# Kernel tuning notes

Hardware: AMD Instinct MI355X
Metric: run time of the kernel (lower is better)

The kernel has to match this reference:

```python
import jax, jax.numpy as jnp
import numpy as np

# Ternary quant: brevitas 2-bit narrow-range signed int quant with const scale 1.0
# -> q(x) = clamp(round(x), -1, 1), values in {-1, 0, 1}

def ternary(x):
    return jnp.clip(jnp.round(x), -1.0, 1.0)

def batchnorm(x, gamma, beta, eps=1e-5):
    # training-mode BatchNorm1d: batch statistics over dim 0 (biased var)
    mean = jnp.mean(x, axis=0)
    var = jnp.var(x, axis=0)
    return (x - mean) * jax.lax.rsqrt(var + eps) * gamma + beta

def tensornorm(x, w, b, eps=1e-4):
    # BNN-PYNQ TensorNorm: normalize over whole tensor (unbiased var), scalar affine
    mean = jnp.mean(x)
    var = jnp.var(x, ddof=1)
    return (x - mean) / jnp.sqrt(var + eps) * w + b


def setup_inputs() -> dict:
    key = jax.random.key(0)
    ks = jax.random.split(key, 4)
    B = 16384
    x = jax.random.uniform(ks[0], (B, 784), dtype=jnp.float32)          # MNIST-like in [0,1]
    W1 = 2.0 * jax.random.uniform(ks[1], (1024, 784), dtype=jnp.float32) - 1.0  # uniform(-1,1)
    W2 = 2.0 * jax.random.uniform(ks[2], (10, 1024), dtype=jnp.float32) - 1.0
    tnk1, tnk2 = jax.random.split(ks[3])
    return {
        "x": x,
        "W1": W1,
        "gamma1": jnp.ones((1024,), jnp.float32),
        "beta1": jnp.zeros((1024,), jnp.float32),
        "W2": W2,
        "gamma2": jnp.ones((10,), jnp.float32),
        "beta2": jnp.zeros((10,), jnp.float32),
        "tn_w": jax.random.uniform(tnk1, (1,), dtype=jnp.float32),
        "tn_b": jax.random.uniform(tnk2, (1,), dtype=jnp.float32),
    }


def reference(x, W1, gamma1, beta1, W2, gamma2, beta2, tn_w, tn_b):
    h = x.reshape(x.shape[0], -1)
    h = 2.0 * h - 1.0                 # input rescale to [-1,1]
    h = ternary(h)                    # QuantIdentity (2-bit act)
    h = h @ ternary(W1).T             # QuantLinear 784->1024, ternary weights, no bias
    h = batchnorm(h, gamma1, beta1)   # BatchNorm1d(1024)
    h = ternary(h)                    # QuantIdentity
    h = h @ ternary(W2).T             # QuantLinear 1024->10
    h = batchnorm(h, gamma2, beta2)   # BatchNorm1d(10)
    h = ternary(h)                    # QuantIdentity
    return tensornorm(h, tn_w, tn_b)  # TensorNorm
```

## Files before the change

### kernel.cpp

```cpp
#include <hip/hip_runtime.h>
#include <stdint.h>

typedef int i32x4 __attribute__((ext_vector_type(4)));
typedef short s16x8 __attribute__((ext_vector_type(8)));
typedef unsigned long long ull;

#define BB 16384
#define KD 784
#define KP 832
#define N1 1024
#define N2 10
#define NTOT (BB * N2)

#define OFF_AQ 0ULL
#define SZ_AQ (13631488ULL)
#define OFF_W1Q (OFF_AQ + SZ_AQ)
#define SZ_W1Q (851968ULL)
#define OFF_W2Q (OFF_W1Q + SZ_W1Q)
#define SZ_W2Q (16384ULL)
#define OFF_C1 (OFF_W2Q + SZ_W2Q)
#define SZ_C1 (33554432ULL)
#define OFF_T8 (OFF_C1 + SZ_C1)
#define SZ_T8 (16777216ULL)
#define OFF_STATS (OFF_T8 + SZ_T8)
#define SZ_STATS (16384ULL)
#define OFF_BN1 (OFF_STATS + SZ_STATS)
#define SZ_BN1 (16384ULL)
#define OFF_C2 (OFF_BN1 + SZ_BN1)
#define SZ_C2 (1048576ULL)
#define OFF_T2 (OFF_C2 + SZ_C2)
#define SZ_T2 (163840ULL)

__device__ __forceinline__ void async16(const void* g, void* l) {
  __builtin_amdgcn_global_load_lds((__attribute__((address_space(1))) void*)(void*)(g),
                                   (__attribute__((address_space(3))) void*)(l), 16, 0, 0);
}

__device__ __forceinline__ int8_t ternq(float v) {
  float q = rintf(v);
  return q > 0.5f ? 1 : (q < -0.5f ? -1 : 0);
}

__global__ void k0_quant(const float* __restrict__ x, const float* __restrict__ W1,
                         const float* __restrict__ W2, int8_t* __restrict__ Aq,
                         int8_t* __restrict__ W1q, int8_t* __restrict__ W2q) {
  const int TA = BB * KP / 16;
  const int TW = N1 * KP / 16;
  const int T2 = N2 * N1 / 16;
  int tid = blockIdx.x * 256 + threadIdx.x;
  union {
    int4 v;
    int8_t b[16];
  } o;
  o.v = make_int4(0, 0, 0, 0);
  if (tid < TA) {
    int base = tid * 16;
    int r = base / KP, k = base - r * KP;
    if (k < KD) {
      const float4* xp = (const float4*)&x[r * KD + k];
#pragma unroll
      for (int g = 0; g < 4; ++g) {
        float4 f = xp[g];
        o.b[g * 4 + 0] = ternq(2.0f * f.x - 1.0f);
        o.b[g * 4 + 1] = ternq(2.0f * f.y - 1.0f);
        o.b[g * 4 + 2] = ternq(2.0f * f.z - 1.0f);
        o.b[g * 4 + 3] = ternq(2.0f * f.w - 1.0f);
      }
    }
    *(int4*)&Aq[base] = o.v;
  } else if (tid < TA + TW) {
    int base = (tid - TA) * 16;
    int r = base / KP, k = base - r * KP;
    if (k < KD) {
      const float4* wp = (const float4*)&W1[r * KD + k];
#pragma unroll
      for (int g = 0; g < 4; ++g) {
        float4 f = wp[g];
        o.b[g * 4 + 0] = ternq(f.x);
        o.b[g * 4 + 1] = ternq(f.y);
        o.b[g * 4 + 2] = ternq(f.z);
        o.b[g * 4 + 3] = ternq(f.w);
      }
    }
    *(int4*)&W1q[base] = o.v;
  } else if (tid < TA + TW + T2) {
    int base = (tid - TA - TW) * 16;
    const float4* wp = (const float4*)&W2[base];
#pragma unroll
    for (int g = 0; g < 4; ++g) {
      float4 f = wp[g];
      o.b[g * 4 + 0] = ternq(f.x);
      o.b[g * 4 + 1] = ternq(f.y);
      o.b[g * 4 + 2] = ternq(f.z);
      o.b[g * 4 + 3] = ternq(f.w);
    }
    *(int4*)&W2q[base] = o.v;
  }
}

__global__ __launch_bounds__(256, 2) void k1_gemm1(const int8_t* __restrict__ Aq,
                                                   const int8_t* __restrict__ W1q,
                                                   short* __restrict__ C1,
                                                   int* __restrict__ colsum,
                                                   ull* __restrict__ colsq) {
  __shared__ int8_t As[128 * 64];
  __shared__ int8_t Bs[128 * 64];
  __shared__ int cS[128];
  __shared__ int cQ[128];
  const int t = threadIdx.x;
  const int lane = t & 63, wave = t >> 6;
  const int wr = wave >> 1, wc = wave & 1;
  const int rowBase = blockIdx.y * 128, colBase = blockIdx.x * 128;
  if (t < 128) {
    cS[t] = 0;
    cQ[t] = 0;
  }

  i32x4 acc[4][4] = {};

  const int r0 = t >> 2;
  const int gsrc = ((t & 3) ^ ((t >> 3) & 3)) * 16;
  const int m = lane & 15;
  const int goff = ((lane >> 4) ^ ((m >> 1) & 3)) * 16;

  for (int kt = 0; kt < KP / 64; ++kt) {
    __syncthreads();
    const int kb = kt * 64;
    async16(&Aq[(size_t)(rowBase + r0) * KP + kb + gsrc], &As[t * 16]);
    async16(&Aq[(size_t)(rowBase + r0 + 64) * KP + kb + gsrc], &As[4096 + t * 16]);
    async16(&W1q[(size_t)(colBase + r0) * KP + kb + gsrc], &Bs[t * 16]);
    async16(&W1q[(size_t)(colBase + r0 + 64) * KP + kb + gsrc], &Bs[4096 + t * 16]);
    __syncthreads();
    i32x4 av[4], bv[4];
#pragma unroll
    for (int i = 0; i < 4; ++i) av[i] = *(const i32x4*)&As[(64 * wr + 16 * i + m) * 64 + goff];
#pragma unroll
    for (int j = 0; j < 4; ++j) bv[j] = *(const i32x4*)&Bs[(64 * wc + 16 * j + m) * 64 + goff];
#pragma unroll
    for (int i = 0; i < 4; ++i)
#pragma unroll
      for (int j = 0; j < 4; ++j)
        acc[i][j] = __builtin_amdgcn_mfma_i32_16x16x64_i8(av[i], bv[j], acc[i][j], 0, 0, 0);
  }

  const int q = lane >> 4, cl = lane & 15;
#pragma unroll
  for (int j = 0; j < 4; ++j) {
    const int colLoc = 64 * wc + 16 * j + cl;
    const int col = colBase + colLoc;
    int s = 0, sq = 0;
#pragma unroll
    for (int i = 0; i < 4; ++i) {
#pragma unroll
      for (int rg = 0; rg < 4; ++rg) {
        int v = acc[i][j][rg];
        int row = rowBase + 64 * wr + 16 * i + q * 4 + rg;
        C1[(size_t)row * N1 + col] = (short)v;
        s += v;
        sq += v * v;
      }
    }
    atomicAdd(&cS[colLoc], s);
    atomicAdd(&cQ[colLoc], sq);
  }
  __syncthreads();
  if (t < 128) {
    atomicAdd(&colsum[colBase + t], cS[t]);
    atomicAdd(&colsq[colBase + t], (ull)(unsigned)cQ[t]);
  }
}

__global__ void k3_bn1(const int* __restrict__ colsum, const ull* __restrict__ colsq,
                       const float* __restrict__ g1, const float* __restrict__ b1,
                       double* __restrict__ Ac, double* __restrict__ Bc) {
  int c = blockIdx.x * 256 + threadIdx.x;
  double mean = (double)colsum[c] / 16384.0;
  double var = (double)colsq[c] / 16384.0 - mean * mean;
  double dinv = 1.0 / sqrt(var + 1e-5);
  double a = dinv * (double)g1[c];
  Ac[c] = a;
  Bc[c] = (double)b1[c] - mean * a;
}

__global__ void k4_bnq(const short* __restrict__ C1, const double* __restrict__ Ac,
                       const double* __restrict__ Bc, int8_t* __restrict__ t8) {
  int id = blockIdx.x * 256 + threadIdx.x;
  int base = id * 8;
  int c0 = base & (N1 - 1);
  s16x8 v = *(const s16x8*)&C1[base];
  union {
    ull u;
    int8_t b[8];
  } o;
#pragma unroll
  for (int u = 0; u < 8; ++u) {
    int c = c0 + u;
    double z = (double)v[u] * Ac[c] + Bc[c];
    double qq = rint(z);
    qq = qq < -1.0 ? -1.0 : (qq > 1.0 ? 1.0 : qq);
    o.b[u] = (int8_t)qq;
  }
  *(ull*)&t8[base] = o.u;
}

__global__ __launch_bounds__(256) void k5_gemm2(const int8_t* __restrict__ t8,
                                                const int8_t* __restrict__ W2q,
                                                int* __restrict__ C2,
                                                int* __restrict__ sum2p,
                                                ull* __restrict__ sq2p) {
  __shared__ int cS[16];
  __shared__ int cQ[16];
  const int t = threadIdx.x;
  if (t < 16) {
    cS[t] = 0;
    cQ[t] = 0;
  }
  const int lane = t & 63, wave = t >> 6;
  const int n = lane & 15, kc = lane >> 4;

  i32x4 bfr[16];
#pragma unroll
  for (int kt = 0; kt < 16; ++kt)
    bfr[kt] = *(const i32x4*)&W2q[n * N1 + kt * 64 + kc * 16];

  const int tile = blockIdx.x * 4 + wave;
  const int rowBase = tile * 16;
  i32x4 acc = {0, 0, 0, 0};
#pragma unroll
  for (int kt = 0; kt < 16; ++kt) {
    i32x4 a = *(const i32x4*)&t8[(size_t)(rowBase + n) * N1 + kt * 64 + kc * 16];
    acc = __builtin_amdgcn_mfma_i32_16x16x64_i8(a, bfr[kt], acc, 0, 0, 0);
  }
  const int col = n;
  int s = 0, sq = 0;
#pragma unroll
  for (int rg = 0; rg < 4; ++rg) {
    int row = rowBase + kc * 4 + rg;
    C2[row * 16 + col] = acc[rg];
  }
  if (col < N2) {
#pragma unroll
    for (int rg = 0; rg < 4; ++rg) {
      int v = acc[rg];
      s += v;
      sq += v * v;
    }
    atomicAdd(&cS[col], s);
    atomicAdd(&cQ[col], sq);
  }
  __syncthreads();
  if (t < N2) {
    atomicAdd(&sum2p[t * 16], cS[t]);
    atomicAdd(&sq2p[t * 8], (ull)(unsigned)cQ[t]);
  }
}

__global__ __launch_bounds__(256) void k7_bn2q(const int* __restrict__ C2,
                                               const int* __restrict__ sum2p,
                                               const ull* __restrict__ sq2p,
                                               const float* __restrict__ g2,
                                               const float* __restrict__ b2,
                                               int8_t* __restrict__ t2, int* __restrict__ gsum,
                                               int* __restrict__ gsq) {
  int s = 0, sq = 0;
  for (int id = blockIdx.x * 256 + threadIdx.x; id < NTOT; id += gridDim.x * 256) {
    int r = id / N2, c = id - r * N2;
    int v = C2[r * 16 + c];
    double mean = (double)sum2p[c * 16] / 16384.0;
    double var = (double)sq2p[c * 8] / 16384.0 - mean * mean;
    double z = ((double)v - mean) / sqrt(var + 1e-5) * (double)g2[c] + (double)b2[c];
    double qq = rint(z);
    qq = qq < -1.0 ? -1.0 : (qq > 1.0 ? 1.0 : qq);
    int ti = (int)qq;
    t2[id] = (int8_t)ti;
    s += ti;
    sq += ti * ti;
  }
#pragma unroll
  for (int off = 32; off > 0; off >>= 1) {
    s += __shfl_xor(s, off, 64);
    sq += __shfl_xor(sq, off, 64);
  }
  __shared__ int bs, bq;
  if (threadIdx.x == 0) {
    bs = 0;
    bq = 0;
  }
  __syncthreads();
  if ((threadIdx.x & 63) == 0) {
    atomicAdd(&bs, s);
    atomicAdd(&bq, sq);
  }
  __syncthreads();
  if (threadIdx.x == 0) {
    atomicAdd(gsum, bs);
    atomicAdd(gsq, bq);
  }
}

__global__ void k9_out(const int8_t* __restrict__ t2, const int* __restrict__ gsum,
                       const int* __restrict__ gsq, const float* __restrict__ tn_w,
                       const float* __restrict__ tn_b, float* __restrict__ out) {
  int id = blockIdx.x * 256 + threadIdx.x;
  double n = (double)NTOT;
  double sm = (double)*gsum;
  double mean = sm / n;
  double var = ((double)*gsq - sm * sm / n) / (n - 1.0);
  double alpha = (double)tn_w[0] / sqrt(var + 1e-4);
  out[id] = (float)(((double)t2[id] - mean) * alpha + (double)tn_b[0]);
}

extern "C" void kernel_launch(void* const* d_in, const int* in_sizes, int n_in, void* d_out,
                              int out_size, void* d_ws, size_t ws_size, hipStream_t stream) {
  const float* x = (const float*)d_in[0];
  const float* W1 = (const float*)d_in[1];
  const float* g1 = (const float*)d_in[2];
  const float* b1 = (const float*)d_in[3];
  const float* W2 = (const float*)d_in[4];
  const float* g2 = (const float*)d_in[5];
  const float* b2 = (const float*)d_in[6];
  const float* tnw = (const float*)d_in[7];
  const float* tnb = (const float*)d_in[8];

  char* ws = (char*)d_ws;
  int8_t* Aq = (int8_t*)(ws + OFF_AQ);
  int8_t* W1q = (int8_t*)(ws + OFF_W1Q);
  int8_t* W2q = (int8_t*)(ws + OFF_W2Q);
  short* C1 = (short*)(ws + OFF_C1);
  int8_t* t8 = (int8_t*)(ws + OFF_T8);
  int* colsum = (int*)(ws + OFF_STATS);
  ull* colsq = (ull*)(ws + OFF_STATS + 4096);
  int* sum2p = (int*)(ws + OFF_STATS + 12288);
  ull* sq2p = (ull*)(ws + OFF_STATS + 13312);
  int* gsum = (int*)(ws + OFF_STATS + 14336);
  int* gsq = (int*)(ws + OFF_STATS + 14400);
  double* Ac = (double*)(ws + OFF_BN1);
  double* Bc = (double*)(ws + OFF_BN1 + 8192);
  int* C2 = (int*)(ws + OFF_C2);
  int8_t* t2 = (int8_t*)(ws + OFF_T2);

  hipMemsetAsync(ws + OFF_STATS, 0, SZ_STATS, stream);

  const int totalT = BB * KP / 16 + N1 * KP / 16 + N2 * N1 / 16;
  k0_quant<<<(totalT + 255) / 256, 256, 0, stream>>>(x, W1, W2, Aq, W1q, W2q);
  k1_gemm1<<<dim3(8, 128), 256, 0, stream>>>(Aq, W1q, C1, colsum, colsq);
  k3_bn1<<<4, 256, 0, stream>>>(colsum, colsq, g1, b1, Ac, Bc);
  k4_bnq<<<BB * N1 / 8 / 256, 256, 0, stream>>>(C1, Ac, Bc, t8);
  k5_gemm2<<<256, 256, 0, stream>>>(t8, W2q, C2, sum2p, sq2p);
  k7_bn2q<<<160, 256, 0, stream>>>(C2, sum2p, sq2p, g2, b2, t2, gsum, gsq);
  k9_out<<<NTOT / 256, 256, 0, stream>>>(t2, gsum, gsq, tnw, tnb, (float*)d_out);
}
```

Measured before the change: 168.3 us.

## Fuse BN1 quantization into GEMM2, fold stats memset into quant kernel

Removes the separate BN1-quantize kernel and its int8 intermediate: GEMM2 now reads the int16 C1 directly, applies the per-column affine and ternary rounding in registers, and feeds the MFMA. Ac/Bc and W2q are staged in LDS per block. The stats memset is folded into k0_quant, and the GEMM1 launch-bounds occupancy hint rises from 2 to 3. This saves a 16MB write plus read and two launches, but GEMM2 now runs only 256 blocks with heavy per-element double math, so it may be latency-bound, and the tighter register budget could cause spills in GEMM1.

```diff
diff --git a/kernel.cpp b/kernel.cpp
--- a/kernel.cpp
+++ b/kernel.cpp
@@ -20,9 +20,7 @@
 #define SZ_W2Q (16384ULL)
 #define OFF_C1 (OFF_W2Q + SZ_W2Q)
 #define SZ_C1 (33554432ULL)
-#define OFF_T8 (OFF_C1 + SZ_C1)
-#define SZ_T8 (16777216ULL)
-#define OFF_STATS (OFF_T8 + SZ_T8)
+#define OFF_STATS (OFF_C1 + SZ_C1)
 #define SZ_STATS (16384ULL)
 #define OFF_BN1 (OFF_STATS + SZ_STATS)
 #define SZ_BN1 (16384ULL)
@@ -43,11 +41,13 @@
 
 __global__ void k0_quant(const float* __restrict__ x, const float* __restrict__ W1,
                          const float* __restrict__ W2, int8_t* __restrict__ Aq,
-                         int8_t* __restrict__ W1q, int8_t* __restrict__ W2q) {
+                         int8_t* __restrict__ W1q, int8_t* __restrict__ W2q,
+                         int* __restrict__ stats) {
   const int TA = BB * KP / 16;
   const int TW = N1 * KP / 16;
   const int T2 = N2 * N1 / 16;
   int tid = blockIdx.x * 256 + threadIdx.x;
+  if (tid < 4096) stats[tid] = 0;
   union {
     int4 v;
     int8_t b[16];
@@ -98,7 +98,7 @@
   }
 }
 
-__global__ __launch_bounds__(256, 2) void k1_gemm1(const int8_t* __restrict__ Aq,
+__global__ __launch_bounds__(256, 3) void k1_gemm1(const int8_t* __restrict__ Aq,
                                                    const int8_t* __restrict__ W1q,
                                                    short* __restrict__ C1,
                                                    int* __restrict__ colsum,
@@ -182,63 +182,70 @@
   Bc[c] = (double)b1[c] - mean * a;
 }
 
-__global__ void k4_bnq(const short* __restrict__ C1, const double* __restrict__ Ac,
-                       const double* __restrict__ Bc, int8_t* __restrict__ t8) {
-  int id = blockIdx.x * 256 + threadIdx.x;
-  int base = id * 8;
-  int c0 = base & (N1 - 1);
-  s16x8 v = *(const s16x8*)&C1[base];
-  union {
-    ull u;
-    int8_t b[8];
-  } o;
-#pragma unroll
-  for (int u = 0; u < 8; ++u) {
-    int c = c0 + u;
-    double z = (double)v[u] * Ac[c] + Bc[c];
-    double qq = rint(z);
-    qq = qq < -1.0 ? -1.0 : (qq > 1.0 ? 1.0 : qq);
-    o.b[u] = (int8_t)qq;
-  }
-  *(ull*)&t8[base] = o.u;
-}
-
-__global__ __launch_bounds__(256) void k5_gemm2(const int8_t* __restrict__ t8,
-                                                const int8_t* __restrict__ W2q,
-                                                int* __restrict__ C2,
-                                                int* __restrict__ sum2p,
-                                                ull* __restrict__ sq2p) {
+#define W2S 1040
+__global__ __launch_bounds__(256) void k45_bnq_gemm2(
+    const short* __restrict__ C1, const double* __restrict__ Ac, const double* __restrict__ Bc,
+    const int8_t* __restrict__ W2q, int* __restrict__ C2, int* __restrict__ sum2p,
+    ull* __restrict__ sq2p) {
+  __shared__ double AcS[N1];
+  __shared__ double BcS[N1];
+  __shared__ int8_t W2s[16 * W2S];
   __shared__ int cS[16];
   __shared__ int cQ[16];
   const int t = threadIdx.x;
+  for (int i = t; i < N1; i += 256) {
+    AcS[i] = Ac[i];
+    BcS[i] = Bc[i];
+  }
+  for (int i = t; i < 1024; i += 256) {
+    int r = i >> 6, c16 = (i & 63) * 16;
+    *(int4*)&W2s[r * W2S + c16] = *(const int4*)&W2q[r * N1 + c16];
+  }
   if (t < 16) {
     cS[t] = 0;
     cQ[t] = 0;
   }
+  __syncthreads();
+
   const int lane = t & 63, wave = t >> 6;
-  const int n = lane & 15, kc = lane >> 4;
-
-  i32x4 bfr[16];
-#pragma unroll
-  for (int kt = 0; kt < 16; ++kt)
-    bfr[kt] = *(const i32x4*)&W2q[n * N1 + kt * 64 + kc * 16];
-
+  const int m = lane & 15, kc = lane >> 4;
   const int tile = blockIdx.x * 4 + wave;
   const int rowBase = tile * 16;
+  const short* arow = &C1[(size_t)(rowBase + m) * N1];
+
   i32x4 acc = {0, 0, 0, 0};
 #pragma unroll
   for (int kt = 0; kt < 16; ++kt) {
-    i32x4 a = *(const i32x4*)&t8[(size_t)(rowBase + n) * N1 + kt * 64 + kc * 16];
-    acc = __builtin_amdgcn_mfma_i32_16x16x64_i8(a, bfr[kt], acc, 0, 0, 0);
-  }
-  const int col = n;
-  int s = 0, sq = 0;
-#pragma unroll
-  for (int rg = 0; rg < 4; ++rg) {
-    int row = rowBase + kc * 4 + rg;
-    C2[row * 16 + col] = acc[rg];
-  }
+    const int k0 = kt * 64 + kc * 16;
+    s16x8 v0 = *(const s16x8*)&arow[k0];
+    s16x8 v1 = *(const s16x8*)&arow[k0 + 8];
+    union {
+      i32x4 v;
+      int8_t b[16];
+    } afr;
+#pragma unroll
+    for (int j = 0; j < 8; ++j) {
+      double z = (double)v0[j] * AcS[k0 + j] + BcS[k0 + j];
+      double qq = rint(z);
+      qq = qq < -1.0 ? -1.0 : (qq > 1.0 ? 1.0 : qq);
+      afr.b[j] = (int8_t)qq;
+    }
+#pragma unroll
+    for (int j = 0; j < 8; ++j) {
+      double z = (double)v1[j] * AcS[k0 + 8 + j] + BcS[k0 + 8 + j];
+      double qq = rint(z);
+      qq = qq < -1.0 ? -1.0 : (qq > 1.0 ? 1.0 : qq);
+      afr.b[8 + j] = (int8_t)qq;
+    }
+    i32x4 bfr = *(const i32x4*)&W2s[m * W2S + k0];
+    acc = __builtin_amdgcn_mfma_i32_16x16x64_i8(afr.v, bfr, acc, 0, 0, 0);
+  }
+
+  const int col = m;
+#pragma unroll
+  for (int rg = 0; rg < 4; ++rg) C2[(rowBase + kc * 4 + rg) * 16 + col] = acc[rg];
   if (col < N2) {
+    int s = 0, sq = 0;
 #pragma unroll
     for (int rg = 0; rg < 4; ++rg) {
       int v = acc[rg];
@@ -327,7 +334,7 @@
   int8_t* W1q = (int8_t*)(ws + OFF_W1Q);
   int8_t* W2q = (int8_t*)(ws + OFF_W2Q);
   short* C1 = (short*)(ws + OFF_C1);
-  int8_t* t8 = (int8_t*)(ws + OFF_T8);
+  int* statsZ = (int*)(ws + OFF_STATS);
   int* colsum = (int*)(ws + OFF_STATS);
   ull* colsq = (ull*)(ws + OFF_STATS + 4096);
   int* sum2p = (int*)(ws + OFF_STATS + 12288);
@@ -339,14 +346,11 @@
   int* C2 = (int*)(ws + OFF_C2);
   int8_t* t2 = (int8_t*)(ws + OFF_T2);
 
-  hipMemsetAsync(ws + OFF_STATS, 0, SZ_STATS, stream);
-
   const int totalT = BB * KP / 16 + N1 * KP / 16 + N2 * N1 / 16;
-  k0_quant<<<(totalT + 255) / 256, 256, 0, stream>>>(x, W1, W2, Aq, W1q, W2q);
+  k0_quant<<<(totalT + 255) / 256, 256, 0, stream>>>(x, W1, W2, Aq, W1q, W2q, statsZ);
   k1_gemm1<<<dim3(8, 128), 256, 0, stream>>>(Aq, W1q, C1, colsum, colsq);
   k3_bn1<<<4, 256, 0, stream>>>(colsum, colsq, g1, b1, Ac, Bc);
-  k4_bnq<<<BB * N1 / 8 / 256, 256, 0, stream>>>(C1, Ac, Bc, t8);
-  k5_gemm2<<<256, 256, 0, stream>>>(t8, W2q, C2, sum2p, sq2p);
+  k45_bnq_gemm2<<<256, 256, 0, stream>>>(C1, Ac, Bc, W2q, C2, sum2p, sq2p);
   k7_bn2q<<<160, 256, 0, stream>>>(C2, sum2p, sq2p, g2, b2, t2, gsum, gsq);
   k9_out<<<NTOT / 256, 256, 0, stream>>>(t2, gsum, gsq, tnw, tnb, (float*)d_out);
 }
```

Result: faster. 157.8 us (-6.2%).
